# Optimization experiments

Hardware: AMD Instinct MI355X
Metric: run time of the kernel (lower is better)

## Reference

```python
import jax, jax.numpy as jnp
import numpy as np

D = 1024
L_COMP = 16384
L_FULL = 32768
EPS = 1e-4


def setup_inputs() -> dict:
    key = jax.random.key(0)
    k1, k2 = jax.random.split(key)
    x = jax.random.normal(k1, (1, L_COMP, D), dtype=jnp.float32)
    p_selected = jax.random.uniform(k2, (L_COMP,), dtype=jnp.float32)
    # boundary mask over full sequence: exactly L_COMP ones, first position forced to 1
    rng = np.random.default_rng(0)
    pos = np.concatenate([[0], np.sort(rng.choice(np.arange(1, L_FULL), L_COMP - 1, replace=False))])
    b_np = np.zeros((1, L_FULL), dtype=np.int32)
    b_np[0, pos] = 1
    b = jnp.asarray(b_np)
    return {"x": x, "p_selected": p_selected, "b": b}


def _ema_scan(x, p):
    # z_t = (1 - p_t) * z_{t-1} + p_t * x_t  (exact math of the mamba chunk scan
    # with A=-1, dt=log(1/(1-p)), B=p, C=1, x pre-divided by dt)
    a = jnp.broadcast_to((1.0 - p)[None, :, None], x.shape)  # (1, L, d) decay
    bxt = p[None, :, None] * x                                # (1, L, d) input term

    def combine(c1, c2):
        a1, b1 = c1
        a2, b2 = c2
        return a1 * a2, a2 * b1 + b2

    _, z = jax.lax.associative_scan(combine, (a, bxt), axis=1)
    return z


def reference(x, p_selected, b):
    p = jnp.clip(p_selected.astype(jnp.float32), EPS, 1.0 - EPS)  # (L_comp,)
    z_bar = _ema_scan(x.astype(jnp.float32), p)                   # (1, L_comp, d)
    plug_back_idx = jnp.cumsum(b, axis=1) - 1                     # (1, L_full)
    out = jnp.take(z_bar[0], plug_back_idx[0], axis=0)[None]      # (1, L_full, d)
    return out.astype(x.dtype)
```

## Files before the change

### kernel.cpp

```cpp
#include <hip/hip_runtime.h>


#define DCH 1024
#define L_COMP 16384
#define L_FULL 32768
#define CHUNK 32
#define NCHUNK (L_COMP / CHUNK)
#define EPSV 1e-4f

__device__ __forceinline__ float clipp(float p) {
    p = fmaxf(p, EPSV);
    p = fminf(p, 1.0f - EPSV);
    return p;
}

__global__ __launch_bounds__(1024) void pos_kernel(const int* __restrict__ b, int* __restrict__ pos) {
    const int tid = threadIdx.x;
    const int lane = tid & 63;
    const int wave = tid >> 6;
    int vals[32];
    const int4* b4 = reinterpret_cast<const int4*>(b) + tid * 8;
#pragma unroll
    for (int j = 0; j < 8; ++j) {
        int4 v = b4[j];
        vals[4 * j + 0] = v.x; vals[4 * j + 1] = v.y;
        vals[4 * j + 2] = v.z; vals[4 * j + 3] = v.w;
    }
    int s = 0;
#pragma unroll
    for (int k = 0; k < 32; ++k) s += vals[k];
    int scan = s;
#pragma unroll
    for (int off = 1; off < 64; off <<= 1) {
        int n = __shfl_up(scan, off, 64);
        if (lane >= off) scan += n;
    }
    __shared__ int wsum[16];
    __shared__ int woff[16];
    if (lane == 63) wsum[wave] = scan;
    __syncthreads();
    if (tid == 0) {
        int acc = 0;
#pragma unroll
        for (int w = 0; w < 16; ++w) { woff[w] = acc; acc += wsum[w]; }
    }
    __syncthreads();
    int idx = woff[wave] + (scan - s);
#pragma unroll
    for (int k = 0; k < 32; ++k) {
        if (vals[k]) pos[idx++] = tid * 32 + k;
    }
    if (tid == 0) pos[L_COMP] = L_FULL;
}

__global__ __launch_bounds__(256) void chunk_kernel(const float* __restrict__ x, const float* __restrict__ p,
                                                    float* __restrict__ Bbuf, float* __restrict__ Abuf) {
    const int c = blockIdx.x;
    const int tid = threadIdx.x;
    const float4* x4 = reinterpret_cast<const float4*>(x) + (size_t)c * CHUNK * (DCH / 4) + tid;
    float4 h = make_float4(0.f, 0.f, 0.f, 0.f);
    float aprod = 1.0f;
    const int base = c * CHUNK;
    for (int ib = 0; ib < CHUNK; ib += 8) {
        float4 xv[8];
        float pv[8];
#pragma unroll
        for (int j = 0; j < 8; ++j) {
            xv[j] = x4[(ib + j) * (DCH / 4)];
            pv[j] = clipp(p[base + ib + j]);
        }
#pragma unroll
        for (int j = 0; j < 8; ++j) {
            float a = 1.0f - pv[j];
            h.x = fmaf(a, h.x, pv[j] * xv[j].x);
            h.y = fmaf(a, h.y, pv[j] * xv[j].y);
            h.z = fmaf(a, h.z, pv[j] * xv[j].z);
            h.w = fmaf(a, h.w, pv[j] * xv[j].w);
            aprod *= a;
        }
    }
    reinterpret_cast<float4*>(Bbuf)[c * (DCH / 4) + tid] = h;
    if (tid == 0) Abuf[c] = aprod;
}

#define BATCHB 32
__global__ __launch_bounds__(64) void interchunk_kernel(const float* __restrict__ Bbuf,
                                                        const float* __restrict__ Abuf,
                                                        float* __restrict__ Hbuf) {
    const int ch = blockIdx.x * 64 + threadIdx.x;
    float h = 0.f;
    for (int cb = 0; cb < NCHUNK; cb += BATCHB) {
        float bv[BATCHB];
        float av[BATCHB];
#pragma unroll
        for (int j = 0; j < BATCHB; ++j) {
            bv[j] = Bbuf[(cb + j) * DCH + ch];
            av[j] = Abuf[cb + j];
        }
#pragma unroll
        for (int j = 0; j < BATCHB; ++j) {
            Hbuf[(cb + j) * DCH + ch] = h;
            h = fmaf(av[j], h, bv[j]);
        }
    }
}

__global__ __launch_bounds__(256) void final_kernel(const float* __restrict__ x, const float* __restrict__ p,
                                                    const float* __restrict__ Hbuf, const int* __restrict__ pos,
                                                    float* __restrict__ out) {
    const int c = blockIdx.x;
    const int tid = threadIdx.x;
    const float4* x4 = reinterpret_cast<const float4*>(x) + (size_t)c * CHUNK * (DCH / 4) + tid;
    float4* out4 = reinterpret_cast<float4*>(out) + tid;
    float4 h = reinterpret_cast<const float4*>(Hbuf)[c * (DCH / 4) + tid];
    const int base = c * CHUNK;
    int f0 = pos[base];
    for (int ib = 0; ib < CHUNK; ib += 8) {
        float4 xv[8];
        float pv[8];
        int fe[8];
#pragma unroll
        for (int j = 0; j < 8; ++j) {
            xv[j] = x4[(ib + j) * (DCH / 4)];
            pv[j] = clipp(p[base + ib + j]);
            fe[j] = pos[base + ib + j + 1];
        }
#pragma unroll
        for (int j = 0; j < 8; ++j) {
            float a = 1.0f - pv[j];
            h.x = fmaf(a, h.x, pv[j] * xv[j].x);
            h.y = fmaf(a, h.y, pv[j] * xv[j].y);
            h.z = fmaf(a, h.z, pv[j] * xv[j].z);
            h.w = fmaf(a, h.w, pv[j] * xv[j].w);
            for (int f = f0; f < fe[j]; ++f) {
                out4[(size_t)f * (DCH / 4)] = h;
            }
            f0 = fe[j];
        }
    }
}

extern "C" void kernel_launch(void* const* d_in, const int* in_sizes, int n_in,
                              void* d_out, int out_size, void* d_ws, size_t ws_size,
                              hipStream_t stream) {
    const float* x = (const float*)d_in[0];
    const float* p = (const float*)d_in[1];
    const int* b = (const int*)d_in[2];
    float* out = (float*)d_out;

    char* ws = (char*)d_ws;
    float* Abuf = (float*)ws;
    int* pos = (int*)(ws + 4096);
    float* Bbuf = (float*)(ws + 4096 + 69632);
    float* Hbuf = Bbuf + (size_t)NCHUNK * DCH;

    pos_kernel<<<1, 1024, 0, stream>>>(b, pos);
    chunk_kernel<<<NCHUNK, 256, 0, stream>>>(x, p, Bbuf, Abuf);
    interchunk_kernel<<<16, 64, 0, stream>>>(Bbuf, Abuf, Hbuf);
    final_kernel<<<NCHUNK, 256, 0, stream>>>(x, p, Hbuf, pos, out);
}
```

Baseline: 235.4 us.

## Fuse position and inter-chunk scans into chunk and dechunk kernels

The single-block position kernel and the 16-block serial inter-chunk kernel are removed, leaving two launches. The chunk kernel now also counts boundary bits per 64-wide segment of b. The dechunk kernel builds a prefix of those counts in shared memory, finds each output position by binary search plus a segment scan, and recomputes its carry-in state by folding all preceding chunk summaries. This gets rid of the serial low-parallelism stages and the Hbuf round trip. The cost is a carry-in pass whose work grows with the chunk index, so the last blocks reread up to about 2 MB of Bbuf, and the added launch bounds may change the register budget.

Result: faster. 226.0 us, median of 2 (-4.0%).

```diff
diff --git a/kernel.cpp b/kernel.cpp
--- a/kernel.cpp
+++ b/kernel.cpp
@@ -6,6 +6,7 @@
 #define L_FULL 32768
 #define CHUNK 32
 #define NCHUNK (L_COMP / CHUNK)
+#define SEG (L_FULL / NCHUNK)
 #define EPSV 1e-4f
 
 __device__ __forceinline__ float clipp(float p) {
@@ -14,53 +15,19 @@
     return p;
 }
 
-__global__ __launch_bounds__(1024) void pos_kernel(const int* __restrict__ b, int* __restrict__ pos) {
+__global__ __launch_bounds__(256, 2) void chunk_kernel(
+    const float* __restrict__ x, const float* __restrict__ p,
+    const int* __restrict__ b,
+    float* __restrict__ Bbuf, float* __restrict__ Abuf, int* __restrict__ bsum) {
+    const int c = blockIdx.x;
     const int tid = threadIdx.x;
     const int lane = tid & 63;
     const int wave = tid >> 6;
-    int vals[32];
-    const int4* b4 = reinterpret_cast<const int4*>(b) + tid * 8;
-#pragma unroll
-    for (int j = 0; j < 8; ++j) {
-        int4 v = b4[j];
-        vals[4 * j + 0] = v.x; vals[4 * j + 1] = v.y;
-        vals[4 * j + 2] = v.z; vals[4 * j + 3] = v.w;
-    }
-    int s = 0;
-#pragma unroll
-    for (int k = 0; k < 32; ++k) s += vals[k];
-    int scan = s;
-#pragma unroll
-    for (int off = 1; off < 64; off <<= 1) {
-        int n = __shfl_up(scan, off, 64);
-        if (lane >= off) scan += n;
-    }
-    __shared__ int wsum[16];
-    __shared__ int woff[16];
-    if (lane == 63) wsum[wave] = scan;
-    __syncthreads();
-    if (tid == 0) {
-        int acc = 0;
-#pragma unroll
-        for (int w = 0; w < 16; ++w) { woff[w] = acc; acc += wsum[w]; }
-    }
-    __syncthreads();
-    int idx = woff[wave] + (scan - s);
-#pragma unroll
-    for (int k = 0; k < 32; ++k) {
-        if (vals[k]) pos[idx++] = tid * 32 + k;
-    }
-    if (tid == 0) pos[L_COMP] = L_FULL;
-}
+    const int base = c * CHUNK;
 
-__global__ __launch_bounds__(256) void chunk_kernel(const float* __restrict__ x, const float* __restrict__ p,
-                                                    float* __restrict__ Bbuf, float* __restrict__ Abuf) {
-    const int c = blockIdx.x;
-    const int tid = threadIdx.x;
     const float4* x4 = reinterpret_cast<const float4*>(x) + (size_t)c * CHUNK * (DCH / 4) + tid;
     float4 h = make_float4(0.f, 0.f, 0.f, 0.f);
     float aprod = 1.0f;
-    const int base = c * CHUNK;
     for (int ib = 0; ib < CHUNK; ib += 8) {
         float4 xv[8];
         float pv[8];
@@ -81,61 +48,132 @@
     }
     reinterpret_cast<float4*>(Bbuf)[c * (DCH / 4) + tid] = h;
     if (tid == 0) Abuf[c] = aprod;
-}
-
-#define BATCHB 32
-__global__ __launch_bounds__(64) void interchunk_kernel(const float* __restrict__ Bbuf,
-                                                        const float* __restrict__ Abuf,
-                                                        float* __restrict__ Hbuf) {
-    const int ch = blockIdx.x * 64 + threadIdx.x;
-    float h = 0.f;
-    for (int cb = 0; cb < NCHUNK; cb += BATCHB) {
-        float bv[BATCHB];
-        float av[BATCHB];
+    if (wave == 0) {
+        int v = b[c * SEG + lane];
+        int s = v;
 #pragma unroll
-        for (int j = 0; j < BATCHB; ++j) {
-            bv[j] = Bbuf[(cb + j) * DCH + ch];
-            av[j] = Abuf[cb + j];
-        }
-#pragma unroll
-        for (int j = 0; j < BATCHB; ++j) {
-            Hbuf[(cb + j) * DCH + ch] = h;
-            h = fmaf(av[j], h, bv[j]);
-        }
+        for (int off = 1; off < 64; off <<= 1) s += __shfl_xor(s, off, 64);
+        if (lane == 0) bsum[c] = s;
     }
 }
 
-__global__ __launch_bounds__(256) void final_kernel(const float* __restrict__ x, const float* __restrict__ p,
-                                                    const float* __restrict__ Hbuf, const int* __restrict__ pos,
-                                                    float* __restrict__ out) {
+__global__ __launch_bounds__(256, 2) void dechunk_kernel(
+    const float* __restrict__ x, const float* __restrict__ p,
+    const int* __restrict__ b, float* __restrict__ out,
+    const float* __restrict__ Bbuf, const float* __restrict__ Abuf,
+    const int* __restrict__ bsum) {
     const int c = blockIdx.x;
     const int tid = threadIdx.x;
-    const float4* x4 = reinterpret_cast<const float4*>(x) + (size_t)c * CHUNK * (DCH / 4) + tid;
-    float4* out4 = reinterpret_cast<float4*>(out) + tid;
-    float4 h = reinterpret_cast<const float4*>(Hbuf)[c * (DCH / 4) + tid];
+    const int lane = tid & 63;
+    const int wave = tid >> 6;
     const int base = c * CHUNK;
-    int f0 = pos[base];
-    for (int ib = 0; ib < CHUNK; ib += 8) {
-        float4 xv[8];
-        float pv[8];
-        int fe[8];
+
+    __shared__ int bpref[NCHUNK + 1];
+    __shared__ int spos[CHUNK + 1];
+    __shared__ int wtot[4];
+
+    {
+        int v0 = bsum[2 * tid];
+        int v1 = bsum[2 * tid + 1];
+        int s = v0 + v1;
+        int incl = s;
 #pragma unroll
-        for (int j = 0; j < 8; ++j) {
-            xv[j] = x4[(ib + j) * (DCH / 4)];
-            pv[j] = clipp(p[base + ib + j]);
-            fe[j] = pos[base + ib + j + 1];
+        for (int off = 1; off < 64; off <<= 1) {
+            int n = __shfl_up(incl, off, 64);
+            if (lane >= off) incl += n;
         }
+        if (lane == 63) wtot[wave] = incl;
+        __syncthreads();
+        int woff = 0;
+        for (int w = 0; w < wave; ++w) woff += wtot[w];
+        int ex = woff + incl - s;
+        bpref[2 * tid] = ex;
+        bpref[2 * tid + 1] = ex + v0;
+        if (tid == 0) bpref[NCHUNK] = L_COMP;
+        __syncthreads();
+    }
+
+    if (tid <= CHUNK) {
+        int t = base + tid;
+        int posv = L_FULL;
+        if (t < L_COMP) {
+            int lo = 0, hi = NCHUNK;
+            while (hi - lo > 1) {
+                int mid = (lo + hi) >> 1;
+                if (bpref[mid] <= t) lo = mid; else hi = mid;
+            }
+            int lr = t - bpref[lo];
+            const int4* bseg = reinterpret_cast<const int4*>(b) + lo * (SEG / 4);
+            int cnt = 0;
+#pragma unroll 4
+            for (int q = 0; q < SEG / 4; ++q) {
+                int4 w = bseg[q];
+                if (w.x) { if (cnt == lr) posv = lo * SEG + 4 * q + 0; ++cnt; }
+                if (w.y) { if (cnt == lr) posv = lo * SEG + 4 * q + 1; ++cnt; }
+                if (w.z) { if (cnt == lr) posv = lo * SEG + 4 * q + 2; ++cnt; }
+                if (w.w) { if (cnt == lr) posv = lo * SEG + 4 * q + 3; ++cnt; }
+            }
+        }
+        spos[tid] = posv;
+    }
+
+    float4 h = make_float4(0.f, 0.f, 0.f, 0.f);
+    {
+        const float4* B4 = reinterpret_cast<const float4*>(Bbuf) + tid;
+        int k = 0;
+        for (; k + 16 <= c; k += 16) {
+            float4 bv[16];
+            float av[16];
 #pragma unroll
-        for (int j = 0; j < 8; ++j) {
-            float a = 1.0f - pv[j];
-            h.x = fmaf(a, h.x, pv[j] * xv[j].x);
-            h.y = fmaf(a, h.y, pv[j] * xv[j].y);
-            h.z = fmaf(a, h.z, pv[j] * xv[j].z);
-            h.w = fmaf(a, h.w, pv[j] * xv[j].w);
-            for (int f = f0; f < fe[j]; ++f) {
-                out4[(size_t)f * (DCH / 4)] = h;
+            for (int j = 0; j < 16; ++j) {
+                bv[j] = B4[(k + j) * (DCH / 4)];
+                av[j] = Abuf[k + j];
             }
-            f0 = fe[j];
+#pragma unroll
+            for (int j = 0; j < 16; ++j) {
+                h.x = fmaf(av[j], h.x, bv[j].x);
+                h.y = fmaf(av[j], h.y, bv[j].y);
+                h.z = fmaf(av[j], h.z, bv[j].z);
+                h.w = fmaf(av[j], h.w, bv[j].w);
+            }
+        }
+        for (; k < c; ++k) {
+            float4 bv = B4[k * (DCH / 4)];
+            float a = Abuf[k];
+            h.x = fmaf(a, h.x, bv.x);
+            h.y = fmaf(a, h.y, bv.y);
+            h.z = fmaf(a, h.z, bv.z);
+            h.w = fmaf(a, h.w, bv.w);
+        }
+    }
+    __syncthreads();
+
+    {
+        const float4* x4 = reinterpret_cast<const float4*>(x) + (size_t)c * CHUNK * (DCH / 4) + tid;
+        float4* out4 = reinterpret_cast<float4*>(out) + tid;
+        int f0 = spos[0];
+        for (int ib = 0; ib < CHUNK; ib += 8) {
+            float4 xv[8];
+            float pv[8];
+            int fe[8];
+#pragma unroll
+            for (int j = 0; j < 8; ++j) {
+                xv[j] = x4[(ib + j) * (DCH / 4)];
+                pv[j] = clipp(p[base + ib + j]);
+                fe[j] = spos[ib + j + 1];
+            }
+#pragma unroll
+            for (int j = 0; j < 8; ++j) {
+                float a = 1.0f - pv[j];
+                h.x = fmaf(a, h.x, pv[j] * xv[j].x);
+                h.y = fmaf(a, h.y, pv[j] * xv[j].y);
+                h.z = fmaf(a, h.z, pv[j] * xv[j].z);
+                h.w = fmaf(a, h.w, pv[j] * xv[j].w);
+                for (int f = f0; f < fe[j]; ++f) {
+                    out4[(size_t)f * (DCH / 4)] = h;
+                }
+                f0 = fe[j];
+            }
         }
     }
 }
@@ -150,12 +188,9 @@
 
     char* ws = (char*)d_ws;
     float* Abuf = (float*)ws;
-    int* pos = (int*)(ws + 4096);
-    float* Bbuf = (float*)(ws + 4096 + 69632);
-    float* Hbuf = Bbuf + (size_t)NCHUNK * DCH;
+    int* bsum = (int*)(ws + 4096);
+    float* Bbuf = (float*)(ws + 8192);
 
-    pos_kernel<<<1, 1024, 0, stream>>>(b, pos);
-    chunk_kernel<<<NCHUNK, 256, 0, stream>>>(x, p, Bbuf, Abuf);
-    interchunk_kernel<<<16, 64, 0, stream>>>(Bbuf, Abuf, Hbuf);
-    final_kernel<<<NCHUNK, 256, 0, stream>>>(x, p, Hbuf, pos, out);
+    chunk_kernel<<<NCHUNK, 256, 0, stream>>>(x, p, b, Bbuf, Abuf, bsum);
+    dechunk_kernel<<<NCHUNK, 256, 0, stream>>>(x, p, b, out, Bbuf, Abuf, bsum);
 }
```
